# Performance work log

Hardware: AMD Instinct MI355X
Metric: run time of the kernel (lower is better)

## Reference

```python
import jax, jax.numpy as jnp
import numpy as np
import math

B, N, C = 2, 1024, 81            # images, proposals per image, classes (incl. background)
IMG_W, IMG_H = 1333, 800         # image size for all images (box.size)
SCORE_THRESH = 0.05
NMS_THRESH = 0.5
DETS_PER_IMG = 100
WX, WY, WW, WH = 10.0, 10.0, 5.0, 5.0   # BoxCoder weights
BBOX_XFORM_CLIP = math.log(1000.0 / 16.0)
NEG_INF = -1e30


def setup_inputs() -> dict:
    key = jax.random.key(0)
    k1, k2, k3, k4 = jax.random.split(key, 4)
    class_logits = jax.random.normal(k1, (B * N, C), dtype=jnp.float32)
    box_regression = jax.random.normal(k2, (B * N, C * 4), dtype=jnp.float32)
    # valid xyxy proposal boxes inside the image
    xy = jax.random.uniform(k3, (B * N, 2), dtype=jnp.float32) * jnp.array([IMG_W - 150.0, IMG_H - 150.0], jnp.float32)
    wh = 10.0 + jax.random.uniform(k4, (B * N, 2), dtype=jnp.float32) * 140.0
    proposal_boxes = jnp.concatenate([xy, xy + wh], axis=-1)
    return {"class_logits": class_logits, "box_regression": box_regression, "proposal_boxes": proposal_boxes}


def box_decode(rel_codes, boxes):
    """BoxCoder.decode (maskrcnn-benchmark). rel_codes [M, 4C], boxes [M,4] xyxy -> [M, C, 4]."""
    TO_REMOVE = 1.0
    widths = boxes[:, 2] - boxes[:, 0] + TO_REMOVE
    heights = boxes[:, 3] - boxes[:, 1] + TO_REMOVE
    ctr_x = boxes[:, 0] + 0.5 * widths
    ctr_y = boxes[:, 1] + 0.5 * heights
    dx = rel_codes[:, 0::4] / WX
    dy = rel_codes[:, 1::4] / WY
    dw = jnp.minimum(rel_codes[:, 2::4] / WW, BBOX_XFORM_CLIP)
    dh = jnp.minimum(rel_codes[:, 3::4] / WH, BBOX_XFORM_CLIP)
    pred_ctr_x = dx * widths[:, None] + ctr_x[:, None]
    pred_ctr_y = dy * heights[:, None] + ctr_y[:, None]
    pred_w = jnp.exp(dw) * widths[:, None]
    pred_h = jnp.exp(dh) * heights[:, None]
    x1 = pred_ctr_x - 0.5 * pred_w
    y1 = pred_ctr_y - 0.5 * pred_h
    x2 = pred_ctr_x + 0.5 * pred_w - 1.0
    y2 = pred_ctr_y + 0.5 * pred_h - 1.0
    return jnp.stack([x1, y1, x2, y2], axis=-1)  # [M, C, 4]


def iou_matrix(b):
    """Pairwise IoU with TO_REMOVE=1 convention. b [N,4] -> [N,N]."""
    area = (b[:, 2] - b[:, 0] + 1.0) * (b[:, 3] - b[:, 1] + 1.0)
    lt = jnp.maximum(b[:, None, :2], b[None, :, :2])
    rb = jnp.minimum(b[:, None, 2:], b[None, :, 2:])
    wh = jnp.clip(rb - lt + 1.0, 0.0)
    inter = wh[..., 0] * wh[..., 1]
    return inter / (area[:, None] + area[None, :] - inter)


def nms_keep(boxes, scores, valid):
    """Masked greedy NMS: returns keep mask [N]. Invalid entries never kept/suppress."""
    s = jnp.where(valid, scores, NEG_INF)
    order = jnp.argsort(-s)            # descending score
    b = boxes[order]
    iou = iou_matrix(b)                # [N, N]
    idx = jnp.arange(N)

    def body(i, keep):
        sup = keep[i] & (iou[i] > NMS_THRESH) & (idx > i)
        return keep & ~sup

    keep_sorted = jax.lax.fori_loop(0, N, body, valid[order])
    return jnp.zeros((N,), bool).at[order].set(keep_sorted)


def per_image(prob, boxes):
    """prob [N,C], boxes [N,C,4] -> top-DETS_PER_IMG (boxes, scores, labels)."""
    fg_prob = prob[:, 1:]              # skip background (cls_start_idx=1)
    fg_boxes = boxes[:, 1:]            # [N, C-1, 4]
    valid = fg_prob > SCORE_THRESH
    # per-class masked NMS, vmapped over the class axis
    keep = jax.vmap(nms_keep, in_axes=(1, 1, 1), out_axes=1)(fg_boxes, fg_prob, valid)  # [N, C-1]
    flat_scores = jnp.where(keep, fg_prob, NEG_INF).reshape(-1)       # [(C-1)*N]
    flat_boxes = fg_boxes.reshape(-1, 4)
    flat_labels = jnp.tile(jnp.arange(1, C, dtype=jnp.int64), (N,))   # matches [N, C-1] flatten
    top_s, top_i = jax.lax.top_k(flat_scores, DETS_PER_IMG)
    valid_top = top_s > SCORE_THRESH
    out_scores = jnp.where(valid_top, top_s, 0.0)
    out_boxes = jnp.where(valid_top[:, None], flat_boxes[top_i], 0.0)
    out_labels = jnp.where(valid_top, flat_labels[top_i], -1)
    return out_boxes, out_scores, out_labels


def reference(class_logits, box_regression, proposal_boxes):
    prob = jax.nn.softmax(class_logits, axis=-1)                # [B*N, C]
    decoded = box_decode(box_regression, proposal_boxes)        # [B*N, C, 4]
    # clip_to_image (remove_empty=False), TO_REMOVE=1
    x = jnp.clip(decoded[..., 0::2], 0.0, IMG_W - 1.0)
    y = jnp.clip(decoded[..., 1::2], 0.0, IMG_H - 1.0)
    decoded = jnp.stack([x[..., 0], y[..., 0], x[..., 1], y[..., 1]], axis=-1)
    prob = prob.reshape(B, N, C)
    decoded = decoded.reshape(B, N, C, 4)
    # process images sequentially to bound the [C-1, N, N] IoU working set
    boxes_out, scores_out, labels_out = jax.lax.map(lambda a: per_image(*a), (prob, decoded))
    return boxes_out, scores_out, labels_out
```

## Files before the change

kernel.cpp:

```cpp
#include <hip/hip_runtime.h>
#include <math.h>

#define B_ 2
#define N_ 1024
#define C_ 81
#define NFG 80
#define DETS 100
#define CAND (N_ * NFG)
#define SCORE_THRESH 0.05f
#define NMS_THRESH 0.5f
#define NEG_INF -1e30f
#define IMG_W_M1 1332.0f
#define IMG_H_M1 799.0f
#define XFORM_CLIP 4.135166556742356f
#define HB 192
#define LCAP 512
#define NROW (B_ * N_)


__device__ __forceinline__ void decode_box(const float* __restrict__ breg,
                                           const float* __restrict__ pbox,
                                           int row, int c, float* out) {
    float bx1 = pbox[row * 4 + 0];
    float by1 = pbox[row * 4 + 1];
    float bx2 = pbox[row * 4 + 2];
    float by2 = pbox[row * 4 + 3];
    float w  = bx2 - bx1 + 1.0f;
    float h  = by2 - by1 + 1.0f;
    float cx = bx1 + 0.5f * w;
    float cy = by1 + 0.5f * h;
    const float* r = breg + (size_t)row * (C_ * 4) + c * 4;
    float dx = r[0] / 10.0f;
    float dy = r[1] / 10.0f;
    float dw = fminf(r[2] / 5.0f, (float)XFORM_CLIP);
    float dh = fminf(r[3] / 5.0f, (float)XFORM_CLIP);
    float px = dx * w + cx;
    float py = dy * h + cy;
    float pw = expf(dw) * w;
    float ph = expf(dh) * h;
    float x1 = px - 0.5f * pw;
    float y1 = py - 0.5f * ph;
    float x2 = px + 0.5f * pw - 1.0f;
    float y2 = py + 0.5f * ph - 1.0f;
    out[0] = fminf(fmaxf(x1, 0.0f), IMG_W_M1);
    out[1] = fminf(fmaxf(y1, 0.0f), IMG_H_M1);
    out[2] = fminf(fmaxf(x2, 0.0f), IMG_W_M1);
    out[3] = fminf(fmaxf(y2, 0.0f), IMG_H_M1);
}


__global__ __launch_bounds__(256) void prob_k(const float* __restrict__ logits,
                                              float* __restrict__ probT,
                                              int* __restrict__ count) {
    if (blockIdx.x == 0 && threadIdx.x < B_) count[threadIdx.x] = 0;
    int row  = blockIdx.x * 4 + (threadIdx.x >> 6);
    int lane = threadIdx.x & 63;
    const float* rp = logits + (size_t)row * C_;
    float v0 = rp[lane];
    float v1 = (lane + 64 < C_) ? rp[lane + 64] : -INFINITY;
    float m = fmaxf(v0, v1);
    #pragma unroll
    for (int off = 32; off; off >>= 1) m = fmaxf(m, __shfl_xor(m, off));
    float e0 = expf(v0 - m);
    float e1 = (lane + 64 < C_) ? expf(v1 - m) : 0.0f;
    float s = e0 + e1;
    #pragma unroll
    for (int off = 32; off; off >>= 1) s += __shfl_xor(s, off);
    probT[(size_t)lane * NROW + row] = e0 / s;
    if (lane + 64 < C_) probT[(size_t)(lane + 64) * NROW + row] = e1 / s;
}


__global__ __launch_bounds__(256) void nms_k(const float* __restrict__ probT,
                                             const float* __restrict__ breg,
                                             const float* __restrict__ pbox,
                                             float* __restrict__ cand_s,
                                             int* __restrict__ cand_i,
                                             int* __restrict__ count) {
    __shared__ float skey[N_];
    __shared__ int   sidx[N_];
    __shared__ float sx1[N_], sy1[N_], sx2[N_], sy2[N_], sar[N_];
    __shared__ unsigned rembits[64];
    __shared__ int   mcount;
    __shared__ float fs[64];  __shared__ int ffi[64];
    __shared__ float fx1[64], fy1[64], fx2[64], fy2[64], far_[64];

    int blk = blockIdx.x;
    int b   = blk / NFG;
    int c   = blk % NFG + 1;
    int tid = threadIdx.x;

    if (tid == 0) mcount = 0;
    __syncthreads();

    const float* col = probT + (size_t)c * NROW + b * N_;
    #pragma unroll
    for (int r = 0; r < N_ / 256; ++r) {
        int n = tid + r * 256;
        float s = col[n];
        if (s > SCORE_THRESH) {
            int p = atomicAdd(&mcount, 1);
            skey[p] = s;
            sidx[p] = n;
        }
    }
    __syncthreads();
    int M = mcount;

    if (M > 0 && M <= 64) {
        if (tid < 64) {
            int lane = tid;
            if (lane < M) {
                float s = skey[lane];
                int idx = sidx[lane];
                int r = 0;
                for (int q = 0; q < M; ++q) {
                    float sq = skey[q]; int iq = sidx[q];
                    if (sq > s || (sq == s && iq < idx)) r++;
                }
                float bx[4];
                decode_box(breg, pbox, b * N_ + idx, c, bx);
                fs[r]  = s;
                ffi[r] = idx;
                fx1[r] = bx[0]; fy1[r] = bx[1]; fx2[r] = bx[2]; fy2[r] = bx[3];
                far_[r] = (bx[2] - bx[0] + 1.0f) * (bx[3] - bx[1] + 1.0f);
            }
        }
        __syncthreads();
        if (tid < 64) {
            int lane = tid;
            bool act = lane < M;
            float s = 0.0f, x1 = 0.f, y1 = 0.f, x2 = 0.f, y2 = 0.f, ar = 0.f;
            int idx = 0;
            if (act) {
                s = fs[lane]; idx = ffi[lane];
                x1 = fx1[lane]; y1 = fy1[lane]; x2 = fx2[lane]; y2 = fy2[lane];
                ar = far_[lane];
            }
            unsigned long long adj = 0ULL;
            for (int i = 0; i < M; ++i) {
                if (act && i < lane) {
                    float xx1 = fmaxf(x1, fx1[i]);
                    float yy1 = fmaxf(y1, fy1[i]);
                    float xx2 = fminf(x2, fx2[i]);
                    float yy2 = fminf(y2, fy2[i]);
                    float w = fmaxf(xx2 - xx1 + 1.0f, 0.0f);
                    float h = fmaxf(yy2 - yy1 + 1.0f, 0.0f);
                    float inter = w * h;
                    float iou = inter / (ar + far_[i] - inter);
                    if (iou > NMS_THRESH) adj |= 1ULL << i;
                }
            }
            int rem = 0;
            for (int i = 0; i < M; ++i) {
                unsigned long long remmask = __ballot(rem != 0);
                if (!((remmask >> i) & 1ULL) && ((adj >> i) & 1ULL)) rem = 1;
            }
            unsigned long long keepmask = __ballot(act && !rem);
            int base = 0;
            if (lane == 0) base = atomicAdd(&count[b], __popcll(keepmask));
            base = __shfl(base, 0);
            if (act && !rem) {
                int pos = base + __popcll(keepmask & ((1ULL << lane) - 1ULL));
                cand_s[(size_t)b * CAND + pos] = s;
                cand_i[(size_t)b * CAND + pos] = idx * NFG + (c - 1);
            }
        }
    } else if (M > 64) {
        int P = 64;
        while (P < M) P <<= 1;
        for (int i = M + tid; i < P; i += 256) { skey[i] = NEG_INF; sidx[i] = 0x7fffffff; }
        __syncthreads();
        for (int k = 2; k <= P; k <<= 1) {
            for (int j = k >> 1; j > 0; j >>= 1) {
                for (int i = tid; i < P; i += 256) {
                    int l = i ^ j;
                    if (l > i) {
                        float ki = skey[i], kl = skey[l];
                        int   ii = sidx[i], il = sidx[l];
                        bool iFirst = (ki > kl) || (ki == kl && ii < il);
                        bool asc = ((i & k) == 0);
                        if (iFirst != asc) {
                            skey[i] = kl; skey[l] = ki;
                            sidx[i] = il; sidx[l] = ii;
                        }
                    }
                }
                __syncthreads();
            }
        }
        for (int i = tid; i < M; i += 256) {
            float box[4];
            decode_box(breg, pbox, b * N_ + sidx[i], c, box);
            sx1[i] = box[0]; sy1[i] = box[1]; sx2[i] = box[2]; sy2[i] = box[3];
            sar[i] = (box[2] - box[0] + 1.0f) * (box[3] - box[1] + 1.0f);
        }
        __syncthreads();
        if (tid < 64) {
            int lane = tid;
            unsigned my = 0;
            for (int i = 0; i < M; ++i) {
                unsigned obits = __shfl(my, i & 63);
                bool kept = ((obits >> (i >> 6)) & 1u) == 0u;
                if (kept) {
                    float x1i = sx1[i], y1i = sy1[i], x2i = sx2[i], y2i = sy2[i], ai = sar[i];
                    for (int j = lane; j < M; j += 64) {
                        if (j > i && !((my >> (j >> 6)) & 1u)) {
                            float xx1 = fmaxf(x1i, sx1[j]);
                            float yy1 = fmaxf(y1i, sy1[j]);
                            float xx2 = fminf(x2i, sx2[j]);
                            float yy2 = fminf(y2i, sy2[j]);
                            float w = fmaxf(xx2 - xx1 + 1.0f, 0.0f);
                            float h = fmaxf(yy2 - yy1 + 1.0f, 0.0f);
                            float inter = w * h;
                            float iou = inter / (ai + sar[j] - inter);
                            if (iou > NMS_THRESH) my |= 1u << (j >> 6);
                        }
                    }
                }
            }
            rembits[lane] = my;
        }
        __syncthreads();
        for (int j = tid; j < M; j += 256) {
            if (!((rembits[j & 63] >> (j >> 6)) & 1u)) {
                int pos = atomicAdd(&count[b], 1);
                cand_s[(size_t)b * CAND + pos] = skey[j];
                cand_i[(size_t)b * CAND + pos] = sidx[j] * NFG + (c - 1);
            }
        }
    }
}


#define TTPB 512

__global__ __launch_bounds__(TTPB) void topk_k(float* __restrict__ cand_s,
                                               const int* __restrict__ cand_i,
                                               const int* __restrict__ count,
                                               const float* __restrict__ breg,
                                               const float* __restrict__ pbox,
                                               float* __restrict__ out) {
    __shared__ int   hist[HB];
    __shared__ int   ssum[HB];
    __shared__ float lsv[LCAP];
    __shared__ int   lfv[LCAP];
    __shared__ int   lcnt;
    __shared__ int   sel_t1;
    __shared__ float rs[TTPB];
    __shared__ int   rf[TTPB];
    __shared__ int   rp[TTPB];

    int b   = blockIdx.x;
    int tid = threadIdx.x;
    int M2  = count[b];
    float* cs = cand_s + (size_t)b * CAND;
    const int* ci = cand_i + (size_t)b * CAND;
    float* boxes_o  = out + (size_t)b * DETS * 4;
    float* scores_o = out + (size_t)B_ * DETS * 4 + (size_t)b * DETS;
    float* labels_o = out + (size_t)B_ * DETS * 4 + (size_t)B_ * DETS + (size_t)b * DETS;

    for (int i = tid; i < HB; i += TTPB) hist[i] = 0;
    if (tid == 0) { lcnt = 0; sel_t1 = 0; }
    __syncthreads();

    for (int i = tid; i < M2; i += TTPB) {
        unsigned bits = __float_as_uint(cs[i]);
        int cb = (int)((bits - 0x3D000000u) >> 18);
        if (cb > HB - 1) cb = HB - 1;
        atomicAdd(&hist[cb], 1);
    }
    __syncthreads();

    if (tid < HB) {
        int acc = 0;
        for (int j = tid; j < HB; ++j) acc += hist[j];
        ssum[tid] = acc;
    }
    __syncthreads();
    if (M2 > DETS && tid < HB) {
        if (ssum[tid] >= DETS && (tid == HB - 1 || ssum[tid + 1] < DETS)) sel_t1 = tid;
    }
    __syncthreads();
    int t1 = sel_t1;

    for (int i = tid; i < M2; i += TTPB) {
        float s = cs[i];
        unsigned bits = __float_as_uint(s);
        int cb = (int)((bits - 0x3D000000u) >> 18);
        if (cb > HB - 1) cb = HB - 1;
        if (cb >= t1) {
            int p = atomicAdd(&lcnt, 1);
            if (p < LCAP) { lsv[p] = s; lfv[p] = ci[i]; }
        }
    }
    __syncthreads();
    int L = lcnt;

    if (L <= LCAP) {
        for (int e = tid; e < L; e += TTPB) {
            float s = lsv[e]; int f = lfv[e];
            int r = 0;
            for (int q = 0; q < L; ++q) {
                float sq = lsv[q]; int fq = lfv[q];
                if (sq > s || (sq == s && fq < f)) r++;
            }
            if (r < DETS) {
                int n = f / NFG;
                int cc = f % NFG + 1;
                float box[4];
                decode_box(breg, pbox, b * N_ + n, cc, box);
                boxes_o[r * 4 + 0] = box[0];
                boxes_o[r * 4 + 1] = box[1];
                boxes_o[r * 4 + 2] = box[2];
                boxes_o[r * 4 + 3] = box[3];
                scores_o[r] = s;
                labels_o[r] = (float)cc;
            }
        }
        int start = (L < DETS) ? L : DETS;
        for (int r = tid; r < DETS; r += TTPB) {
            if (r >= start) {
                boxes_o[r * 4 + 0] = 0.0f;
                boxes_o[r * 4 + 1] = 0.0f;
                boxes_o[r * 4 + 2] = 0.0f;
                boxes_o[r * 4 + 3] = 0.0f;
                scores_o[r] = 0.0f;
                labels_o[r] = -1.0f;
            }
        }
    } else {
        for (int it = 0; it < DETS; ++it) {
            float bs = NEG_INF; int bf = 0x7fffffff; int bp = -1;
            for (int i = tid; i < M2; i += TTPB) {
                float s = cs[i]; int f = ci[i];
                if (s > bs || (s == bs && f < bf)) { bs = s; bf = f; bp = i; }
            }
            rs[tid] = bs; rf[tid] = bf; rp[tid] = bp;
            __syncthreads();
            for (int off = TTPB / 2; off; off >>= 1) {
                if (tid < off) {
                    if (rs[tid + off] > rs[tid] ||
                        (rs[tid + off] == rs[tid] && rf[tid + off] < rf[tid])) {
                        rs[tid] = rs[tid + off]; rf[tid] = rf[tid + off]; rp[tid] = rp[tid + off];
                    }
                }
                __syncthreads();
            }
            if (tid == 0) {
                float s = rs[0];
                bool valid = s > SCORE_THRESH;
                float box[4] = {0.f, 0.f, 0.f, 0.f};
                float lab = -1.0f, scv = 0.0f;
                if (valid) {
                    int fi = rf[0];
                    int n = fi / NFG;
                    int cc = fi % NFG + 1;
                    decode_box(breg, pbox, b * N_ + n, cc, box);
                    lab = (float)cc; scv = s;
                    cs[rp[0]] = NEG_INF;
                }
                boxes_o[it * 4 + 0] = box[0];
                boxes_o[it * 4 + 1] = box[1];
                boxes_o[it * 4 + 2] = box[2];
                boxes_o[it * 4 + 3] = box[3];
                scores_o[it] = scv;
                labels_o[it] = lab;
            }
            __syncthreads();
        }
    }
}


extern "C" void kernel_launch(void* const* d_in, const int* in_sizes, int n_in,
                              void* d_out, int out_size, void* d_ws, size_t ws_size,
                              hipStream_t stream) {
    const float* logits = (const float*)d_in[0];
    const float* breg   = (const float*)d_in[1];
    const float* pbox   = (const float*)d_in[2];
    float* out = (float*)d_out;

    float* cand_s = (float*)d_ws;
    int*   cand_i = (int*)(cand_s + (size_t)B_ * CAND);
    int*   count  = (int*)(cand_i + (size_t)B_ * CAND);
    float* probT  = (float*)(count + 2);

    prob_k<<<NROW / 4, 256, 0, stream>>>(logits, probT, count);
    nms_k<<<B_ * NFG, 256, 0, stream>>>(probT, breg, pbox, cand_s, cand_i, count);
    topk_k<<<B_, TTPB, 0, stream>>>(cand_s, cand_i, count, breg, pbox, out);
}
```

Before: 40.30 us.

## Fuse top-k into NMS kernel via last-block-done atomic counter

Merges the per-image top-k kernel into the per-class NMS kernel. Each block atomically increments a per-image done counter after a threadfence, and the last block for each image runs the histogram and top-k selection. This removes one kernel launch and its gap. The top-k now runs with 256 threads instead of 512, and the shared memory per block grows. The change also skips writing the unused background-class probability row.

```diff
diff --git a/kernel.cpp b/kernel.cpp
--- a/kernel.cpp
+++ b/kernel.cpp
@@ -16,6 +16,7 @@
 #define HB 192
 #define LCAP 512
 #define NROW (B_ * N_)
+#define TPB 256
 
 
 __device__ __forceinline__ void decode_box(const float* __restrict__ breg,
@@ -51,8 +52,9 @@
 
 __global__ __launch_bounds__(256) void prob_k(const float* __restrict__ logits,
                                               float* __restrict__ probT,
-                                              int* __restrict__ count) {
-    if (blockIdx.x == 0 && threadIdx.x < B_) count[threadIdx.x] = 0;
+                                              int* __restrict__ count,
+                                              int* __restrict__ done) {
+    if (blockIdx.x == 0 && threadIdx.x < B_) { count[threadIdx.x] = 0; done[threadIdx.x] = 0; }
     int row  = blockIdx.x * 4 + (threadIdx.x >> 6);
     int lane = threadIdx.x & 63;
     const float* rp = logits + (size_t)row * C_;
@@ -66,24 +68,36 @@
     float s = e0 + e1;
     #pragma unroll
     for (int off = 32; off; off >>= 1) s += __shfl_xor(s, off);
-    probT[(size_t)lane * NROW + row] = e0 / s;
+    if (lane != 0) probT[(size_t)lane * NROW + row] = e0 / s;
     if (lane + 64 < C_) probT[(size_t)(lane + 64) * NROW + row] = e1 / s;
 }
 
 
-__global__ __launch_bounds__(256) void nms_k(const float* __restrict__ probT,
-                                             const float* __restrict__ breg,
-                                             const float* __restrict__ pbox,
-                                             float* __restrict__ cand_s,
-                                             int* __restrict__ cand_i,
-                                             int* __restrict__ count) {
+__global__ __launch_bounds__(TPB) void nms_topk_k(const float* __restrict__ probT,
+                                                  const float* __restrict__ breg,
+                                                  const float* __restrict__ pbox,
+                                                  float* __restrict__ cand_s,
+                                                  int* __restrict__ cand_i,
+                                                  int* __restrict__ count,
+                                                  int* __restrict__ done,
+                                                  float* __restrict__ out) {
     __shared__ float skey[N_];
     __shared__ int   sidx[N_];
     __shared__ float sx1[N_], sy1[N_], sx2[N_], sy2[N_], sar[N_];
     __shared__ unsigned rembits[64];
     __shared__ int   mcount;
+    __shared__ int   is_last;
     __shared__ float fs[64];  __shared__ int ffi[64];
     __shared__ float fx1[64], fy1[64], fx2[64], fy2[64], far_[64];
+    __shared__ int   hist[HB];
+    __shared__ int   ssum[HB];
+    __shared__ float lsv[LCAP];
+    __shared__ int   lfv[LCAP];
+    __shared__ int   lcnt;
+    __shared__ int   sel_t1;
+    __shared__ float rs[TPB];
+    __shared__ int   rf[TPB];
+    __shared__ int   rp[TPB];
 
     int blk = blockIdx.x;
     int b   = blk / NFG;
@@ -95,8 +109,8 @@
 
     const float* col = probT + (size_t)c * NROW + b * N_;
     #pragma unroll
-    for (int r = 0; r < N_ / 256; ++r) {
-        int n = tid + r * 256;
+    for (int r = 0; r < N_ / TPB; ++r) {
+        int n = tid + r * TPB;
         float s = col[n];
         if (s > SCORE_THRESH) {
             int p = atomicAdd(&mcount, 1);
@@ -169,11 +183,11 @@
     } else if (M > 64) {
         int P = 64;
         while (P < M) P <<= 1;
-        for (int i = M + tid; i < P; i += 256) { skey[i] = NEG_INF; sidx[i] = 0x7fffffff; }
+        for (int i = M + tid; i < P; i += TPB) { skey[i] = NEG_INF; sidx[i] = 0x7fffffff; }
         __syncthreads();
         for (int k = 2; k <= P; k <<= 1) {
             for (int j = k >> 1; j > 0; j >>= 1) {
-                for (int i = tid; i < P; i += 256) {
+                for (int i = tid; i < P; i += TPB) {
                     int l = i ^ j;
                     if (l > i) {
                         float ki = skey[i], kl = skey[l];
@@ -189,7 +203,7 @@
                 __syncthreads();
             }
         }
-        for (int i = tid; i < M; i += 256) {
+        for (int i = tid; i < M; i += TPB) {
             float box[4];
             decode_box(breg, pbox, b * N_ + sidx[i], c, box);
             sx1[i] = box[0]; sy1[i] = box[1]; sx2[i] = box[2]; sy2[i] = box[3];
@@ -222,7 +236,7 @@
             rembits[lane] = my;
         }
         __syncthreads();
-        for (int j = tid; j < M; j += 256) {
+        for (int j = tid; j < M; j += TPB) {
             if (!((rembits[j & 63] >> (j >> 6)) & 1u)) {
                 int pos = atomicAdd(&count[b], 1);
                 cand_s[(size_t)b * CAND + pos] = skey[j];
@@ -230,41 +244,29 @@
             }
         }
     }
-}
-
-
-#define TTPB 512
-
-__global__ __launch_bounds__(TTPB) void topk_k(float* __restrict__ cand_s,
-                                               const int* __restrict__ cand_i,
-                                               const int* __restrict__ count,
-                                               const float* __restrict__ breg,
-                                               const float* __restrict__ pbox,
-                                               float* __restrict__ out) {
-    __shared__ int   hist[HB];
-    __shared__ int   ssum[HB];
-    __shared__ float lsv[LCAP];
-    __shared__ int   lfv[LCAP];
-    __shared__ int   lcnt;
-    __shared__ int   sel_t1;
-    __shared__ float rs[TTPB];
-    __shared__ int   rf[TTPB];
-    __shared__ int   rp[TTPB];
-
-    int b   = blockIdx.x;
-    int tid = threadIdx.x;
-    int M2  = count[b];
+
+    __syncthreads();
+    if (tid == 0) {
+        __threadfence();
+        int t = atomicAdd(&done[b], 1);
+        is_last = (t == NFG - 1) ? 1 : 0;
+    }
+    __syncthreads();
+    if (!is_last) return;
+    __threadfence();
+
+    int M2 = count[b];
     float* cs = cand_s + (size_t)b * CAND;
     const int* ci = cand_i + (size_t)b * CAND;
     float* boxes_o  = out + (size_t)b * DETS * 4;
     float* scores_o = out + (size_t)B_ * DETS * 4 + (size_t)b * DETS;
     float* labels_o = out + (size_t)B_ * DETS * 4 + (size_t)B_ * DETS + (size_t)b * DETS;
 
-    for (int i = tid; i < HB; i += TTPB) hist[i] = 0;
+    for (int i = tid; i < HB; i += TPB) hist[i] = 0;
     if (tid == 0) { lcnt = 0; sel_t1 = 0; }
     __syncthreads();
 
-    for (int i = tid; i < M2; i += TTPB) {
+    for (int i = tid; i < M2; i += TPB) {
         unsigned bits = __float_as_uint(cs[i]);
         int cb = (int)((bits - 0x3D000000u) >> 18);
         if (cb > HB - 1) cb = HB - 1;
@@ -284,7 +286,7 @@
     __syncthreads();
     int t1 = sel_t1;
 
-    for (int i = tid; i < M2; i += TTPB) {
+    for (int i = tid; i < M2; i += TPB) {
         float s = cs[i];
         unsigned bits = __float_as_uint(s);
         int cb = (int)((bits - 0x3D000000u) >> 18);
@@ -298,7 +300,7 @@
     int L = lcnt;
 
     if (L <= LCAP) {
-        for (int e = tid; e < L; e += TTPB) {
+        for (int e = tid; e < L; e += TPB) {
             float s = lsv[e]; int f = lfv[e];
             int r = 0;
             for (int q = 0; q < L; ++q) {
@@ -319,7 +321,7 @@
             }
         }
         int start = (L < DETS) ? L : DETS;
-        for (int r = tid; r < DETS; r += TTPB) {
+        for (int r = tid; r < DETS; r += TPB) {
             if (r >= start) {
                 boxes_o[r * 4 + 0] = 0.0f;
                 boxes_o[r * 4 + 1] = 0.0f;
@@ -332,13 +334,13 @@
     } else {
         for (int it = 0; it < DETS; ++it) {
             float bs = NEG_INF; int bf = 0x7fffffff; int bp = -1;
-            for (int i = tid; i < M2; i += TTPB) {
+            for (int i = tid; i < M2; i += TPB) {
                 float s = cs[i]; int f = ci[i];
                 if (s > bs || (s == bs && f < bf)) { bs = s; bf = f; bp = i; }
             }
             rs[tid] = bs; rf[tid] = bf; rp[tid] = bp;
             __syncthreads();
-            for (int off = TTPB / 2; off; off >>= 1) {
+            for (int off = TPB / 2; off; off >>= 1) {
                 if (tid < off) {
                     if (rs[tid + off] > rs[tid] ||
                         (rs[tid + off] == rs[tid] && rf[tid + off] < rf[tid])) {
@@ -384,9 +386,10 @@
     float* cand_s = (float*)d_ws;
     int*   cand_i = (int*)(cand_s + (size_t)B_ * CAND);
     int*   count  = (int*)(cand_i + (size_t)B_ * CAND);
-    float* probT  = (float*)(count + 2);
-
-    prob_k<<<NROW / 4, 256, 0, stream>>>(logits, probT, count);
-    nms_k<<<B_ * NFG, 256, 0, stream>>>(probT, breg, pbox, cand_s, cand_i, count);
-    topk_k<<<B_, TTPB, 0, stream>>>(cand_s, cand_i, count, breg, pbox, out);
+    int*   done   = count + B_;
+    float* probT  = (float*)(done + B_);
+
+    prob_k<<<NROW / 4, 256, 0, stream>>>(logits, probT, count, done);
+    nms_topk_k<<<B_ * NFG, TPB, 0, stream>>>(probT, breg, pbox, cand_s, cand_i,
+                                             count, done, out);
 }
```

New measurement: 41.52 us. 3.1% more time.
